# Optimization experiments

Hardware: AMD Instinct MI355X
Metric: run time of the kernel (lower is better)

Reference implementation:

```python
import jax, jax.numpy as jnp
import numpy as np

T, C, H, N = 1024, 2048, 32, 64
D_LORA, D_G = 64, 128

def _ln(x, w, b, eps=1e-5):
    m = x.mean(-1, keepdims=True)
    v = ((x - m) ** 2).mean(-1, keepdims=True)
    return (x - m) * jax.lax.rsqrt(v + eps) * w + b

def setup_inputs():
    key = jax.random.key(0)
    ks = iter(jax.random.split(key, 48))
    rn = lambda shape, s=1.0: jax.random.normal(next(ks), shape, dtype=jnp.float32) * s
    return {
        "x": rn((T, C)),
        "x_prev_att": rn((C,)),
        "vk_state": rn((H, N, N), 0.1),
        "x_prev_ffn": rn((C,)),
        "v_first": rn((T, C)),
        "ln1_w": jnp.ones((C,), jnp.float32), "ln1_b": jnp.zeros((C,), jnp.float32),
        "x_r": rn((C,), 0.1), "x_w": rn((C,), 0.1), "x_k": rn((C,), 0.1),
        "x_v": rn((C,), 0.1), "x_a": rn((C,), 0.1), "x_g": rn((C,), 0.1),
        "w0": rn((C,), 0.1), "w1": rn((C, D_LORA), 0.02), "w2": rn((D_LORA, C), 0.02),
        "a0": rn((C,), 0.1), "a1": rn((C, D_LORA), 0.02), "a2": rn((D_LORA, C), 0.02),
        "v0": rn((C,), 0.1), "v1": rn((C, D_LORA), 0.02), "v2": rn((D_LORA, C), 0.02),
        "g1": rn((C, D_G), 0.02), "g2": rn((D_G, C), 0.02),
        "k_k": rn((C,), 0.1), "k_a": rn((C,), 0.1), "r_k": rn((C,), 0.1),
        "R_": rn((C, C), 0.02), "K_": rn((C, C), 0.02),
        "V_": rn((C, C), 0.02), "O_": rn((C, C), 0.02),
        "lnx_w": jnp.ones((C,), jnp.float32), "lnx_b": jnp.zeros((C,), jnp.float32),
        "ln2_w": jnp.ones((C,), jnp.float32), "ln2_b": jnp.zeros((C,), jnp.float32),
        "ffn_x_k": rn((C,), 0.1),
        "ffn_K": rn((C, 4 * C), 0.02), "ffn_V": rn((4 * C, C), 0.02),
    }

def reference(x, x_prev_att, vk_state, x_prev_ffn, v_first, ln1_w, ln1_b,
              x_r, x_w, x_k, x_v, x_a, x_g, w0, w1, w2, a0, a1, a2,
              v0, v1, v2, g1, g2, k_k, k_a, r_k, R_, K_, V_, O_,
              lnx_w, lnx_b, ln2_w, ln2_b, ffn_x_k, ffn_K, ffn_V):
    # ---- TMix: RWKV-7 time mixing (layer_id = 1, so v_first blend is active) ----
    xln = _ln(x, ln1_w, ln1_b)                                  # [T, C]
    dx = jnp.concatenate([x_prev_att[None, :], xln[:-1]], axis=0) - xln  # token shift
    xr, xw, xk, xv, xa, xg = (xln + dx * m for m in (x_r, x_w, x_k, x_v, x_a, x_g))
    r = xr @ R_
    w = jnp.tanh(xw @ w1) @ w2
    k = xk @ K_
    v = xv @ V_
    a = jax.nn.sigmoid(a0 + (xa @ a1) @ a2)
    g = jax.nn.sigmoid(xg @ g1) @ g2
    kk = (k * k_k).reshape(T, H, N)
    kk = kk / jnp.maximum(jnp.linalg.norm(kk, axis=-1, keepdims=True), 1e-12)  # L2 normalize per head
    k = k * (1.0 + (a - 1.0) * k_a)
    v = v + (v_first - v) * jax.nn.sigmoid(v0 + (xv @ v1) @ v2)  # layer_id != 0 path
    w = jnp.exp(-0.606531 * jax.nn.sigmoid(w0 + w))               # per-channel decay in (0,1)
    rh, kh, vh = r.reshape(T, H, N), k.reshape(T, H, N), v.reshape(T, H, N)
    ah, wh = a.reshape(T, H, N), w.reshape(T, H, N)

    def step(state, inp):
        # state: [H, N, N]; generalized delta rule: state*w + state@(-kk)(kk*a)^T + v k^T
        w_t, kk_t, a_t, k_t, v_t, r_t = inp
        ab = jnp.einsum('hi,hj->hij', -kk_t, kk_t * a_t)
        vk = jnp.einsum('hi,hj->hij', v_t, k_t)
        state = state * w_t[:, None, :] + jnp.einsum('hij,hjk->hik', state, ab) + vk
        return state, jnp.einsum('hij,hj->hi', state, r_t)

    vk_state, outs = jax.lax.scan(step, vk_state, (wh, kk, ah, kh, vh, rh))  # outs: [T, H, N]
    # group norm over H groups, eps = 0.00064, affine per-channel
    m = outs.mean(-1, keepdims=True)
    var = ((outs - m) ** 2).mean(-1, keepdims=True)
    gn = ((outs - m) * jax.lax.rsqrt(var + 0.00064)).reshape(T, C) * lnx_w + lnx_b
    bonus = ((r * k * r_k).reshape(T, H, N).sum(-1, keepdims=True) * vh).reshape(T, C)
    x = x + ((gn + bonus) * g) @ O_
    # ---- CMix: gated squared-ReLU MLP ----
    xln2 = _ln(x, ln2_w, ln2_b)
    dx2 = jnp.concatenate([x_prev_ffn[None, :], xln2[:-1]], axis=0) - xln2
    kf = jax.nn.relu((xln2 + dx2 * ffn_x_k) @ ffn_K) ** 2
    x = x + kf @ ffn_V
    return x
```

## Files before the change

kernel.cpp:

```cpp
#include <hip/hip_runtime.h>
#include <hip/hip_bf16.h>


#define T_ 1024
#define C_ 2048
#define H_ 32
#define NH 64

typedef __attribute__((ext_vector_type(8))) short short8v;
typedef __attribute__((ext_vector_type(4))) float f32x4;

__device__ __forceinline__ float bf2f(unsigned short u) {
  union { float f; unsigned int i; } c; c.i = ((unsigned int)u) << 16; return c.f;
}
__device__ __forceinline__ unsigned short f2bf(float f) {
  union { float f; unsigned int i; } c; c.f = f;
  unsigned int x = c.i;
  return (unsigned short)((x + 0x7fffu + ((x >> 16) & 1u)) >> 16);
}
__device__ __forceinline__ float sigm(float x) { return 1.f / (1.f + __expf(-x)); }

__device__ __forceinline__ void load8bf(const unsigned short* p, float* o) {
  union { int4 v; unsigned short u[8]; } c;
  c.v = *(const int4*)p;
#pragma unroll
  for (int i = 0; i < 8; ++i) o[i] = bf2f(c.u[i]);
}
__device__ __forceinline__ void store8bf(unsigned short* p, const float* o) {
  union { int4 v; unsigned short u[8]; } c;
#pragma unroll
  for (int i = 0; i < 8; ++i) c.u[i] = f2bf(o[i]);
  *(int4*)p = c.v;
}
__device__ __forceinline__ void load8f(const float* p, float* o) {
  float4 a = ((const float4*)p)[0], b = ((const float4*)p)[1];
  o[0] = a.x; o[1] = a.y; o[2] = a.z; o[3] = a.w;
  o[4] = b.x; o[5] = b.y; o[6] = b.z; o[7] = b.w;
}
__device__ __forceinline__ void load4f(const float* p, float* o) {
  float4 a = *(const float4*)p;
  o[0] = a.x; o[1] = a.y; o[2] = a.z; o[3] = a.w;
}

#define GLD16(g, l)                                                        \
  __builtin_amdgcn_global_load_lds(                                        \
      (const __attribute__((address_space(1))) void*)(g),                  \
      (__attribute__((address_space(3))) void*)(l), 16, 0, 0)

__global__ __launch_bounds__(256) void lnmix6_kernel(
    const float* __restrict__ x, const float* __restrict__ xprev,
    const float* __restrict__ lw, const float* __restrict__ lb,
    const float* __restrict__ mr, const float* __restrict__ mw,
    const float* __restrict__ mk, const float* __restrict__ mv,
    const float* __restrict__ ma, const float* __restrict__ mg,
    unsigned short* xr, unsigned short* xw, unsigned short* xk,
    unsigned short* xv, unsigned short* xa, unsigned short* xg) {
  int t = blockIdx.x, tid = threadIdx.x, c = tid * 8;
  float cur[8], prv[8];
  load8f(x + (size_t)t * C_ + c, cur);
  if (t == 0) load8f(xprev + c, prv);
  else load8f(x + (size_t)(t - 1) * C_ + c, prv);
  float sc = 0.f, qc = 0.f, sp = 0.f, qp = 0.f;
#pragma unroll
  for (int i = 0; i < 8; ++i) {
    sc += cur[i]; qc += cur[i] * cur[i];
    sp += prv[i]; qp += prv[i] * prv[i];
  }
  for (int m = 1; m < 64; m <<= 1) {
    sc += __shfl_xor(sc, m); qc += __shfl_xor(qc, m);
    sp += __shfl_xor(sp, m); qp += __shfl_xor(qp, m);
  }
  __shared__ float r4[4][4];
  if ((tid & 63) == 0) {
    r4[tid >> 6][0] = sc; r4[tid >> 6][1] = qc;
    r4[tid >> 6][2] = sp; r4[tid >> 6][3] = qp;
  }
  __syncthreads();
  sc = r4[0][0] + r4[1][0] + r4[2][0] + r4[3][0];
  qc = r4[0][1] + r4[1][1] + r4[2][1] + r4[3][1];
  sp = r4[0][2] + r4[1][2] + r4[2][2] + r4[3][2];
  qp = r4[0][3] + r4[1][3] + r4[2][3] + r4[3][3];
  float mc = sc * (1.f / C_);
  float rc = rsqrtf(qc * (1.f / C_) - mc * mc + 1e-5f);
  float mp = sp * (1.f / C_);
  float rp = rsqrtf(qp * (1.f / C_) - mp * mp + 1e-5f);
  float cw[8], cb[8];
  load8f(lw + c, cw); load8f(lb + c, cb);
  float curn[8], prvn[8];
#pragma unroll
  for (int i = 0; i < 8; ++i) {
    curn[i] = (cur[i] - mc) * rc * cw[i] + cb[i];
    prvn[i] = (t == 0) ? prv[i] : (prv[i] - mp) * rp * cw[i] + cb[i];
  }
  float cf[8], o[8];
  const float* coefs[6] = {mr, mw, mk, mv, ma, mg};
  unsigned short* outs6[6] = {xr, xw, xk, xv, xa, xg};
#pragma unroll
  for (int a = 0; a < 6; ++a) {
    load8f(coefs[a] + c, cf);
#pragma unroll
    for (int i = 0; i < 8; ++i) o[i] = curn[i] + (prvn[i] - curn[i]) * cf[i];
    store8bf(outs6[a] + (size_t)t * C_ + c, o);
  }
}

__global__ __launch_bounds__(256) void lnmix1_kernel(
    const float* __restrict__ x, const float* __restrict__ xprev,
    const float* __restrict__ lw, const float* __restrict__ lb,
    const float* __restrict__ coef, unsigned short* __restrict__ out) {
  int t = blockIdx.x, tid = threadIdx.x, c = tid * 8;
  float cur[8], prv[8];
  load8f(x + (size_t)t * C_ + c, cur);
  if (t == 0) load8f(xprev + c, prv);
  else load8f(x + (size_t)(t - 1) * C_ + c, prv);
  float sc = 0.f, qc = 0.f, sp = 0.f, qp = 0.f;
#pragma unroll
  for (int i = 0; i < 8; ++i) {
    sc += cur[i]; qc += cur[i] * cur[i];
    sp += prv[i]; qp += prv[i] * prv[i];
  }
  for (int m = 1; m < 64; m <<= 1) {
    sc += __shfl_xor(sc, m); qc += __shfl_xor(qc, m);
    sp += __shfl_xor(sp, m); qp += __shfl_xor(qp, m);
  }
  __shared__ float r4[4][4];
  if ((tid & 63) == 0) {
    r4[tid >> 6][0] = sc; r4[tid >> 6][1] = qc;
    r4[tid >> 6][2] = sp; r4[tid >> 6][3] = qp;
  }
  __syncthreads();
  sc = r4[0][0] + r4[1][0] + r4[2][0] + r4[3][0];
  qc = r4[0][1] + r4[1][1] + r4[2][1] + r4[3][1];
  sp = r4[0][2] + r4[1][2] + r4[2][2] + r4[3][2];
  qp = r4[0][3] + r4[1][3] + r4[2][3] + r4[3][3];
  float mc = sc * (1.f / C_);
  float rc = rsqrtf(qc * (1.f / C_) - mc * mc + 1e-5f);
  float mp = sp * (1.f / C_);
  float rp = rsqrtf(qp * (1.f / C_) - mp * mp + 1e-5f);
  float cw[8], cb[8], cf[8], o[8];
  load8f(lw + c, cw); load8f(lb + c, cb); load8f(coef + c, cf);
#pragma unroll
  for (int i = 0; i < 8; ++i) {
    float cn = (cur[i] - mc) * rc * cw[i] + cb[i];
    float pn = (t == 0) ? prv[i] : (prv[i] - mp) * rp * cw[i] + cb[i];
    o[i] = cn + (pn - cn) * cf[i];
  }
  store8bf(out + (size_t)t * C_ + c, o);
}

__global__ __launch_bounds__(256) void transpose_kernel(
    const float* in0, const float* in1, const float* in2,
    unsigned short* o0, unsigned short* o1, unsigned short* o2,
    int R, int Cc) {
  const float* in = blockIdx.z == 0 ? in0 : (blockIdx.z == 1 ? in1 : in2);
  unsigned short* out = blockIdx.z == 0 ? o0 : (blockIdx.z == 1 ? o1 : o2);
  __shared__ __align__(16) unsigned short tile[64][80];
  int c0 = blockIdx.x * 64, r0 = blockIdx.y * 64;
  int rr = threadIdx.x >> 4, cq = threadIdx.x & 15;
#pragma unroll
  for (int i = 0; i < 4; ++i) {
    int r = rr + i * 16;
    float4 v = *(const float4*)(in + (size_t)(r0 + r) * Cc + c0 + cq * 4);
    tile[cq * 4 + 0][r] = f2bf(v.x);
    tile[cq * 4 + 1][r] = f2bf(v.y);
    tile[cq * 4 + 2][r] = f2bf(v.z);
    tile[cq * 4 + 3][r] = f2bf(v.w);
  }
  __syncthreads();
  int cr = threadIdx.x >> 2, rg = threadIdx.x & 3;
  int4 w0 = *(const int4*)&tile[cr][rg * 16];
  int4 w1 = *(const int4*)&tile[cr][rg * 16 + 8];
  unsigned short* op = out + (size_t)(c0 + cr) * R + r0 + rg * 16;
  *(int4*)op = w0;
  *(int4*)(op + 8) = w1;
}

template <int EPI>
__global__ __launch_bounds__(256) void gemm2_kernel(
    const unsigned short* A0, const unsigned short* A1, const unsigned short* A2,
    const unsigned short* B0, const unsigned short* B1, const unsigned short* B2,
    void* C0, void* C1, void* C2, const float* __restrict__ addsrc,
    int M, int K, int N) {
  int z = blockIdx.z;
  const unsigned short* A = z == 0 ? A0 : (z == 1 ? A1 : A2);
  const unsigned short* Bt = z == 0 ? B0 : (z == 1 ? B1 : B2);
  void* Cout = z == 0 ? C0 : (z == 1 ? C1 : C2);
  __shared__ __align__(16) unsigned short As[2][128 * 32];
  __shared__ __align__(16) unsigned short Bs[2][128 * 32];
  const int tid = threadIdx.x, lane = tid & 63, wid = tid >> 6;
  const int bm = blockIdx.y * 128, bn = blockIdx.x * 128;
  const int wr = wid >> 1, wc = wid & 1;
  const int mrow = lane & 15, krow = lane >> 4;
  auto stage = [&](int buf, int kt) {
#pragma unroll
    for (int q = 0; q < 2; ++q) {
      int s = q * 2048 + tid * 8;
      int m = s >> 5, k = s & 31;
      GLD16(A + (size_t)(bm + m) * K + kt + k, &As[buf][s]);
      GLD16(Bt + (size_t)(bn + m) * K + kt + k, &Bs[buf][s]);
    }
  };
  f32x4 acc[4][4] = {};
  stage(0, 0);
  __syncthreads();
  int buf = 0;
  for (int kt = 0; kt < K; kt += 32) {
    if (kt + 32 < K) stage(buf ^ 1, kt + 32);
    short8v af[4], bfrag[4];
#pragma unroll
    for (int i = 0; i < 4; ++i)
      af[i] = *(const short8v*)&As[buf][(wr * 64 + i * 16 + mrow) * 32 + krow * 8];
#pragma unroll
    for (int j = 0; j < 4; ++j)
      bfrag[j] = *(const short8v*)&Bs[buf][(wc * 64 + j * 16 + mrow) * 32 + krow * 8];
#pragma unroll
    for (int i = 0; i < 4; ++i)
#pragma unroll
      for (int j = 0; j < 4; ++j)
        acc[i][j] = __builtin_amdgcn_mfma_f32_16x16x32_bf16(af[i], bfrag[j], acc[i][j], 0, 0, 0);
    __syncthreads();
    buf ^= 1;
  }
#pragma unroll
  for (int i = 0; i < 4; ++i)
#pragma unroll
    for (int j = 0; j < 4; ++j)
#pragma unroll
      for (int e = 0; e < 4; ++e) {
        int grow = bm + wr * 64 + i * 16 + (lane >> 4) * 4 + e;
        int gcol = bn + wc * 64 + j * 16 + (lane & 15);
        size_t off = (size_t)grow * N + gcol;
        float v = acc[i][j][e];
        if constexpr (EPI == 0) ((float*)Cout)[off] = v;
        else if constexpr (EPI == 1) ((float*)Cout)[off] = addsrc[off] + v;
        else { float r = v > 0.f ? v : 0.f; ((unsigned short*)Cout)[off] = f2bf(r * r); }
      }
}

__global__ __launch_bounds__(256) void gemm2ks_kernel(
    const unsigned short* __restrict__ A, const unsigned short* __restrict__ Bt,
    unsigned short* __restrict__ P, int M, int KH, int Ktot, int N) {
  int kz = blockIdx.z;
  const size_t kbase = (size_t)kz * KH;
  __shared__ __align__(16) unsigned short As[2][128 * 32];
  __shared__ __align__(16) unsigned short Bs[2][128 * 32];
  const int tid = threadIdx.x, lane = tid & 63, wid = tid >> 6;
  const int bm = blockIdx.y * 128, bn = blockIdx.x * 128;
  const int wr = wid >> 1, wc = wid & 1;
  const int mrow = lane & 15, krow = lane >> 4;
  auto stage = [&](int buf, int kt) {
#pragma unroll
    for (int q = 0; q < 2; ++q) {
      int s = q * 2048 + tid * 8;
      int m = s >> 5, k = s & 31;
      GLD16(A + (size_t)(bm + m) * Ktot + kbase + kt + k, &As[buf][s]);
      GLD16(Bt + (size_t)(bn + m) * Ktot + kbase + kt + k, &Bs[buf][s]);
    }
  };
  f32x4 acc[4][4] = {};
  stage(0, 0);
  __syncthreads();
  int buf = 0;
  for (int kt = 0; kt < KH; kt += 32) {
    if (kt + 32 < KH) stage(buf ^ 1, kt + 32);
    short8v af[4], bfrag[4];
#pragma unroll
    for (int i = 0; i < 4; ++i)
      af[i] = *(const short8v*)&As[buf][(wr * 64 + i * 16 + mrow) * 32 + krow * 8];
#pragma unroll
    for (int j = 0; j < 4; ++j)
      bfrag[j] = *(const short8v*)&Bs[buf][(wc * 64 + j * 16 + mrow) * 32 + krow * 8];
#pragma unroll
    for (int i = 0; i < 4; ++i)
#pragma unroll
      for (int j = 0; j < 4; ++j)
        acc[i][j] = __builtin_amdgcn_mfma_f32_16x16x32_bf16(af[i], bfrag[j], acc[i][j], 0, 0, 0);
    __syncthreads();
    buf ^= 1;
  }
  unsigned short* Pz = P + (size_t)kz * M * N;
#pragma unroll
  for (int i = 0; i < 4; ++i)
#pragma unroll
    for (int j = 0; j < 4; ++j)
#pragma unroll
      for (int e = 0; e < 4; ++e) {
        int grow = bm + wr * 64 + i * 16 + (lane >> 4) * 4 + e;
        int gcol = bn + wc * 64 + j * 16 + (lane & 15);
        Pz[(size_t)grow * N + gcol] = f2bf(acc[i][j][e]);
      }
}

__global__ __launch_bounds__(256) void gemm2ks3_kernel(
    const unsigned short* A0, const unsigned short* A1, const unsigned short* A2,
    const unsigned short* B0, const unsigned short* B1, const unsigned short* B2,
    unsigned short* __restrict__ P, int M, int KH, int Ktot, int N) {
  int z = blockIdx.z;
  int batch = z % 3, kz = z / 3;
  const unsigned short* A = batch == 0 ? A0 : (batch == 1 ? A1 : A2);
  const unsigned short* Bt = batch == 0 ? B0 : (batch == 1 ? B1 : B2);
  const size_t kbase = (size_t)kz * KH;
  __shared__ __align__(16) unsigned short As[2][128 * 32];
  __shared__ __align__(16) unsigned short Bs[2][128 * 32];
  const int tid = threadIdx.x, lane = tid & 63, wid = tid >> 6;
  const int bm = blockIdx.y * 128, bn = blockIdx.x * 128;
  const int wr = wid >> 1, wc = wid & 1;
  const int mrow = lane & 15, krow = lane >> 4;
  auto stage = [&](int buf, int kt) {
#pragma unroll
    for (int q = 0; q < 2; ++q) {
      int s = q * 2048 + tid * 8;
      int m = s >> 5, k = s & 31;
      GLD16(A + (size_t)(bm + m) * Ktot + kbase + kt + k, &As[buf][s]);
      GLD16(Bt + (size_t)(bn + m) * Ktot + kbase + kt + k, &Bs[buf][s]);
    }
  };
  f32x4 acc[4][4] = {};
  stage(0, 0);
  __syncthreads();
  int buf = 0;
  for (int kt = 0; kt < KH; kt += 32) {
    if (kt + 32 < KH) stage(buf ^ 1, kt + 32);
    short8v af[4], bfrag[4];
#pragma unroll
    for (int i = 0; i < 4; ++i)
      af[i] = *(const short8v*)&As[buf][(wr * 64 + i * 16 + mrow) * 32 + krow * 8];
#pragma unroll
    for (int j = 0; j < 4; ++j)
      bfrag[j] = *(const short8v*)&Bs[buf][(wc * 64 + j * 16 + mrow) * 32 + krow * 8];
#pragma unroll
    for (int i = 0; i < 4; ++i)
#pragma unroll
      for (int j = 0; j < 4; ++j)
        acc[i][j] = __builtin_amdgcn_mfma_f32_16x16x32_bf16(af[i], bfrag[j], acc[i][j], 0, 0, 0);
    __syncthreads();
    buf ^= 1;
  }
  unsigned short* Pz = P + (size_t)z * M * N;
#pragma unroll
  for (int i = 0; i < 4; ++i)
#pragma unroll
    for (int j = 0; j < 4; ++j)
#pragma unroll
      for (int e = 0; e < 4; ++e) {
        int grow = bm + wr * 64 + i * 16 + (lane >> 4) * 4 + e;
        int gcol = bn + wc * 64 + j * 16 + (lane & 15);
        Pz[(size_t)grow * N + gcol] = f2bf(acc[i][j][e]);
      }
}

__global__ __launch_bounds__(256) void add5_kernel(
    const float* __restrict__ a, const unsigned short* __restrict__ p,
    float* __restrict__ o) {
  size_t i = ((size_t)blockIdx.x * 256 + threadIdx.x) * 8;
  const size_t TC = (size_t)T_ * C_;
  float va[8], v0[8], v1[8], v2[8], v3[8], r[8];
  load8f(a + i, va);
  load8bf(p + i, v0);
  load8bf(p + i + TC, v1);
  load8bf(p + i + 2 * TC, v2);
  load8bf(p + i + 3 * TC, v3);
#pragma unroll
  for (int k = 0; k < 8; ++k) r[k] = va[k] + v0[k] + v1[k] + v2[k] + v3[k];
  *(float4*)(o + i) = make_float4(r[0], r[1], r[2], r[3]);
  *(float4*)(o + i + 4) = make_float4(r[4], r[5], r[6], r[7]);
}

__global__ __launch_bounds__(256) void gemm_ks3_kernel(
    const unsigned short* A0, const unsigned short* A1, const unsigned short* A2,
    const unsigned short* B0, const unsigned short* B1, const unsigned short* B2,
    float* P0, float* P1, float* P2, int K, int N) {
  int mz = blockIdx.z >> 3, kz = blockIdx.z & 7;
  const unsigned short* A = mz == 0 ? A0 : (mz == 1 ? A1 : A2);
  const unsigned short* Bt = mz == 0 ? B0 : (mz == 1 ? B1 : B2);
  float* partial = mz == 0 ? P0 : (mz == 1 ? P1 : P2);
  __shared__ __align__(16) unsigned short As[2][128 * 32];
  __shared__ __align__(16) unsigned short Bs[2][64 * 32];
  const int tid = threadIdx.x, lane = tid & 63, wid = tid >> 6;
  const int bn = blockIdx.x * 64, bm = blockIdx.y * 128;
  const int wr = wid >> 1, wc = wid & 1;
  const int mrow = lane & 15, krow = lane >> 4;
  auto stage = [&](int buf, int kt) {
#pragma unroll
    for (int q = 0; q < 2; ++q) {
      int s = q * 2048 + tid * 8;
      int m = s >> 5, k = s & 31;
      GLD16(A + (size_t)(bm + m) * K + kt + k, &As[buf][s]);
    }
    {
      int s = tid * 8;
      int n = s >> 5, k = s & 31;
      GLD16(Bt + (size_t)(bn + n) * K + kt + k, &Bs[buf][s]);
    }
  };
  f32x4 acc[4][2] = {};
  int k0 = kz * 256;
  stage(0, k0);
  __syncthreads();
  int buf = 0;
  for (int kt = k0; kt < k0 + 256; kt += 32) {
    if (kt + 32 < k0 + 256) stage(buf ^ 1, kt + 32);
    short8v af[4], bfrag[2];
#pragma unroll
    for (int i = 0; i < 4; ++i)
      af[i] = *(const short8v*)&As[buf][(wr * 64 + i * 16 + mrow) * 32 + krow * 8];
#pragma unroll
    for (int j = 0; j < 2; ++j)
      bfrag[j] = *(const short8v*)&Bs[buf][(wc * 32 + j * 16 + mrow) * 32 + krow * 8];
#pragma unroll
    for (int i = 0; i < 4; ++i)
#pragma unroll
      for (int j = 0; j < 2; ++j)
        acc[i][j] = __builtin_amdgcn_mfma_f32_16x16x32_bf16(af[i], bfrag[j], acc[i][j], 0, 0, 0);
    __syncthreads();
    buf ^= 1;
  }
#pragma unroll
  for (int i = 0; i < 4; ++i)
#pragma unroll
    for (int j = 0; j < 2; ++j)
#pragma unroll
      for (int e = 0; e < 4; ++e) {
        int row = bm + wr * 64 + i * 16 + (lane >> 4) * 4 + e;
        int col = bn + wc * 32 + j * 16 + (lane & 15);
        partial[((size_t)kz * 1024 + row) * N + col] = acc[i][j][e];
      }
}

__global__ __launch_bounds__(256) void gemm_ks_kernel(
    const unsigned short* __restrict__ A, const unsigned short* __restrict__ Bt,
    float* __restrict__ partial, int K, int N) {
  __shared__ __align__(16) unsigned short As[2][128 * 32];
  __shared__ __align__(16) unsigned short Bs[2][64 * 32];
  const int tid = threadIdx.x, lane = tid & 63, wid = tid >> 6;
  const int bn = blockIdx.x * 64, bm = blockIdx.y * 128, kz = blockIdx.z;
  const int wr = wid >> 1, wc = wid & 1;
  const int mrow = lane & 15, krow = lane >> 4;
  auto stage = [&](int buf, int kt) {
#pragma unroll
    for (int q = 0; q < 2; ++q) {
      int s = q * 2048 + tid * 8;
      int m = s >> 5, k = s & 31;
      GLD16(A + (size_t)(bm + m) * K + kt + k, &As[buf][s]);
    }
    {
      int s = tid * 8;
      int n = s >> 5, k = s & 31;
      GLD16(Bt + (size_t)(bn + n) * K + kt + k, &Bs[buf][s]);
    }
  };
  f32x4 acc[4][2] = {};
  int k0 = kz * 256;
  stage(0, k0);
  __syncthreads();
  int buf = 0;
  for (int kt = k0; kt < k0 + 256; kt += 32) {
    if (kt + 32 < k0 + 256) stage(buf ^ 1, kt + 32);
    short8v af[4], bfrag[2];
#pragma unroll
    for (int i = 0; i < 4; ++i)
      af[i] = *(const short8v*)&As[buf][(wr * 64 + i * 16 + mrow) * 32 + krow * 8];
#pragma unroll
    for (int j = 0; j < 2; ++j)
      bfrag[j] = *(const short8v*)&Bs[buf][(wc * 32 + j * 16 + mrow) * 32 + krow * 8];
#pragma unroll
    for (int i = 0; i < 4; ++i)
#pragma unroll
      for (int j = 0; j < 2; ++j)
        acc[i][j] = __builtin_amdgcn_mfma_f32_16x16x32_bf16(af[i], bfrag[j], acc[i][j], 0, 0, 0);
    __syncthreads();
    buf ^= 1;
  }
#pragma unroll
  for (int i = 0; i < 4; ++i)
#pragma unroll
    for (int j = 0; j < 2; ++j)
#pragma unroll
      for (int e = 0; e < 4; ++e) {
        int row = bm + wr * 64 + i * 16 + (lane >> 4) * 4 + e;
        int col = bn + wc * 32 + j * 16 + (lane & 15);
        partial[((size_t)kz * 1024 + row) * N + col] = acc[i][j][e];
      }
}

__global__ __launch_bounds__(128) void lora_combine_kernel(
    const float* __restrict__ pw, const float* __restrict__ pa,
    const float* __restrict__ pv, const float* __restrict__ pg,
    unsigned short* __restrict__ hw, unsigned short* __restrict__ ha,
    unsigned short* __restrict__ hv, unsigned short* __restrict__ hg) {
  int t = blockIdx.x, which = blockIdx.y, tid = threadIdx.x;
  int Nl = (which == 3) ? 128 : 64;
  if (tid >= Nl) return;
  const float* p = which == 0 ? pw : which == 1 ? pa : which == 2 ? pv : pg;
  float s = 0.f;
#pragma unroll
  for (int kz = 0; kz < 8; ++kz) s += p[((size_t)kz * 1024 + t) * Nl + tid];
  float r = which == 0 ? tanhf(s) : (which == 3 ? sigm(s) : s);
  unsigned short* o = which == 0 ? hw : which == 1 ? ha : which == 2 ? hv : hg;
  o[t * Nl + tid] = f2bf(r);
}

__global__ __launch_bounds__(256) void post_kernel(
    const unsigned short* __restrict__ qRKV, const float* __restrict__ wpre,
    const float* __restrict__ apre, const float* __restrict__ vpre,
    const float* __restrict__ vfirst, const float* __restrict__ w0,
    const float* __restrict__ a0, const float* __restrict__ v0_,
    const float* __restrict__ k_k, const float* __restrict__ k_a,
    float* __restrict__ scanin) {
  int t = blockIdx.x, tid = threadIdx.x;
  int c = tid * 8, h = tid >> 3, j = c & 63;
  size_t o = (size_t)t * C_ + c;
  const size_t TC = (size_t)T_ * C_;
  float rv[8], kv[8], vv[8], t0[8], wv[8], av[8], vp[8], vf[8];
  load8bf(qRKV + o, rv);          load8bf(qRKV + 3 * TC + o, t0);
#pragma unroll
  for (int i = 0; i < 8; ++i) rv[i] += t0[i];
  load8bf(qRKV + TC + o, kv);     load8bf(qRKV + 4 * TC + o, t0);
#pragma unroll
  for (int i = 0; i < 8; ++i) kv[i] += t0[i];
  load8bf(qRKV + 2 * TC + o, vv); load8bf(qRKV + 5 * TC + o, t0);
#pragma unroll
  for (int i = 0; i < 8; ++i) vv[i] += t0[i];
  load8f(wpre + o, wv); load8f(apre + o, av); load8f(vpre + o, vp);
  load8f(vfirst + o, vf);
  float ckk[8], cka[8], cw0[8], ca0[8], cv0[8];
  load8f(k_k + c, ckk); load8f(k_a + c, cka); load8f(w0 + c, cw0);
  load8f(a0 + c, ca0); load8f(v0_ + c, cv0);
  float kk[8]; float ss = 0.f;
#pragma unroll
  for (int i = 0; i < 8; ++i) { kk[i] = kv[i] * ckk[i]; ss += kk[i] * kk[i]; }
  ss += __shfl_xor(ss, 1); ss += __shfl_xor(ss, 2); ss += __shfl_xor(ss, 4);
  float rdn = 1.f / fmaxf(sqrtf(ss), 1e-12f);
  float sw[8], skn[8], scc[8], sk2[8], sv[8];
#pragma unroll
  for (int i = 0; i < 8; ++i) {
    float kkn = kk[i] * rdn;
    float a = sigm(ca0[i] + av[i]);
    skn[i] = kkn;
    scc[i] = -kkn * a;
    sk2[i] = kv[i] * (1.f + (a - 1.f) * cka[i]);
    float sg = sigm(cv0[i] + vp[i]);
    sv[i] = vv[i] + (vf[i] - vv[i]) * sg;
    sw[i] = __expf(-0.606531f * sigm(cw0[i] + wv[i]));
  }
  float* bp = scanin + ((size_t)h * T_ + t) * 384 + j;
  ((float4*)(bp + 0))[0]   = make_float4(sw[0], sw[1], sw[2], sw[3]);
  ((float4*)(bp + 4))[0]   = make_float4(sw[4], sw[5], sw[6], sw[7]);
  ((float4*)(bp + 64))[0]  = make_float4(skn[0], skn[1], skn[2], skn[3]);
  ((float4*)(bp + 68))[0]  = make_float4(skn[4], skn[5], skn[6], skn[7]);
  ((float4*)(bp + 128))[0] = make_float4(scc[0], scc[1], scc[2], scc[3]);
  ((float4*)(bp + 132))[0] = make_float4(scc[4], scc[5], scc[6], scc[7]);
  ((float4*)(bp + 192))[0] = make_float4(sk2[0], sk2[1], sk2[2], sk2[3]);
  ((float4*)(bp + 196))[0] = make_float4(sk2[4], sk2[5], sk2[6], sk2[7]);
  ((float4*)(bp + 256))[0] = make_float4(sv[0], sv[1], sv[2], sv[3]);
  ((float4*)(bp + 260))[0] = make_float4(sv[4], sv[5], sv[6], sv[7]);
  ((float4*)(bp + 320))[0] = make_float4(rv[0], rv[1], rv[2], rv[3]);
  ((float4*)(bp + 324))[0] = make_float4(rv[4], rv[5], rv[6], rv[7]);
}

struct SR { float wv[4], nv[4], cv[4], kv[4], rv[4], vvv; };

template <int CTRL>
__device__ __forceinline__ float dppadd(float x) {
  int y = __builtin_amdgcn_update_dpp(0, __float_as_int(x), CTRL, 0xF, 0xF, true);
  return x + __int_as_float(y);
}
__device__ __forceinline__ float red16(float x) {
  x = dppadd<0xB1>(x);
  x = dppadd<0x4E>(x);
  x = dppadd<0x140>(x);
  x = dppadd<0x141>(x);
  return x;
}

__device__ __forceinline__ void loadstep(const float* S, SR& R, int p4, int row) {
  load4f(S + p4, R.wv);
  load4f(S + 64 + p4, R.nv);
  load4f(S + 128 + p4, R.cv);
  load4f(S + 192 + p4, R.kv);
  load4f(S + 320 + p4, R.rv);
  R.vvv = S[256 + row];
}

__device__ __forceinline__ void stepcomp(const SR& R, float* st, int part,
                                         float* __restrict__ ob, size_t oidx) {
  float p0 = fmaf(st[0], R.nv[0], 0.f);
  float p1 = fmaf(st[1], R.nv[1], 0.f);
  p0 = fmaf(st[2], R.nv[2], p0);
  p1 = fmaf(st[3], R.nv[3], p1);
  float sa = red16(p0 + p1);
  float s0 = 0.f, s1 = 0.f;
#pragma unroll
  for (int i = 0; i < 4; ++i) {
    float t = fmaf(st[i], R.wv[i], fmaf(sa, R.cv[i], R.vvv * R.kv[i]));
    st[i] = t;
    if (i & 1) s1 = fmaf(t, R.rv[i], s1);
    else s0 = fmaf(t, R.rv[i], s0);
  }
  float so = red16(s0 + s1);
  if (part == 0) ob[oidx] = so;
}

__global__ __launch_bounds__(64) void scan5_kernel(
    const float* __restrict__ scanin, const float* __restrict__ vk0,
    float* __restrict__ outs) {
  int bid = blockIdx.x;
  int h = (bid & 7) + 8 * ((bid >> 3) & 3);
  int rg = bid >> 5;
  int tid = threadIdx.x;
  int part = tid & 15, row = rg * 4 + (tid >> 4);
  int p4 = part * 4;
  float st[4];
  load4f(vk0 + ((size_t)h * NH + row) * NH + p4, st);
  const float* src = scanin + (size_t)h * T_ * 384;
  float* ob = outs + h * NH + row;
  SR A, B, C, D;
  loadstep(src + 0 * 384, A, p4, row);
  loadstep(src + 1 * 384, B, p4, row);
  loadstep(src + 2 * 384, C, p4, row);
  int s = 0;
  for (; s < T_ - 4; s += 4) {
    const float* sp = src + (size_t)s * 384;
    loadstep(sp + 3 * 384, D, p4, row);
    stepcomp(A, st, part, ob, (size_t)(s + 0) * C_);
    loadstep(sp + 4 * 384, A, p4, row);
    stepcomp(B, st, part, ob, (size_t)(s + 1) * C_);
    loadstep(sp + 5 * 384, B, p4, row);
    stepcomp(C, st, part, ob, (size_t)(s + 2) * C_);
    loadstep(sp + 6 * 384, C, p4, row);
    stepcomp(D, st, part, ob, (size_t)(s + 3) * C_);
  }
  loadstep(src + (size_t)(T_ - 1) * 384, D, p4, row);
  stepcomp(A, st, part, ob, (size_t)(s + 0) * C_);
  stepcomp(B, st, part, ob, (size_t)(s + 1) * C_);
  stepcomp(C, st, part, ob, (size_t)(s + 2) * C_);
  stepcomp(D, st, part, ob, (size_t)(s + 3) * C_);
}

__global__ __launch_bounds__(256) void gnb_kernel(
    const float* __restrict__ outs, const float* __restrict__ scanin,
    const float* __restrict__ g, const float* __restrict__ rk,
    const float* __restrict__ gw, const float* __restrict__ gb,
    unsigned short* __restrict__ attin) {
  int t = blockIdx.x, tid = threadIdx.x;
  int c = tid * 8, h = tid >> 3, j = c & 63;
  float o[8], gv[8], rkv[8];
  load8f(outs + (size_t)t * C_ + c, o);
  load8f(g + (size_t)t * C_ + c, gv);
  load8f(rk + c, rkv);
  size_t sbase = ((size_t)h * T_ + t) * 384 + j;
  float rv[8], k2[8], vv[8];
  load8f(scanin + sbase + 320, rv);
  load8f(scanin + sbase + 192, k2);
  load8f(scanin + sbase + 256, vv);
  float s = 0.f, q = 0.f, bs = 0.f;
#pragma unroll
  for (int i = 0; i < 8; ++i) {
    s += o[i]; q += o[i] * o[i];
    bs += rv[i] * k2[i] * rkv[i];
  }
  s += __shfl_xor(s, 1); s += __shfl_xor(s, 2); s += __shfl_xor(s, 4);
  q += __shfl_xor(q, 1); q += __shfl_xor(q, 2); q += __shfl_xor(q, 4);
  bs += __shfl_xor(bs, 1); bs += __shfl_xor(bs, 2); bs += __shfl_xor(bs, 4);
  float mean = s * (1.f / NH);
  float var = q * (1.f / NH) - mean * mean;
  float rstd = rsqrtf(var + 0.00064f);
  float res[8];
#pragma unroll
  for (int i = 0; i < 8; ++i) {
    float gn = (o[i] - mean) * rstd * gw[c + i] + gb[c + i];
    res[i] = (gn + bs * vv[i]) * gv[i];
  }
  store8bf(attin + (size_t)t * C_ + c, res);
}

extern "C" void kernel_launch(void* const* d_in, const int* in_sizes, int n_in,
                              void* d_out, int out_size, void* d_ws, size_t ws_size,
                              hipStream_t stream) {
  const float* x       = (const float*)d_in[0];
  const float* xprev_a = (const float*)d_in[1];
  const float* vk0     = (const float*)d_in[2];
  const float* xprev_f = (const float*)d_in[3];
  const float* vfirst  = (const float*)d_in[4];
  const float* ln1w = (const float*)d_in[5];
  const float* ln1b = (const float*)d_in[6];
  const float* m_r = (const float*)d_in[7];
  const float* m_w = (const float*)d_in[8];
  const float* m_k = (const float*)d_in[9];
  const float* m_v = (const float*)d_in[10];
  const float* m_a = (const float*)d_in[11];
  const float* m_g = (const float*)d_in[12];
  const float* w0 = (const float*)d_in[13];
  const float* w1 = (const float*)d_in[14];
  const float* w2 = (const float*)d_in[15];
  const float* a0 = (const float*)d_in[16];
  const float* a1 = (const float*)d_in[17];
  const float* a2 = (const float*)d_in[18];
  const float* v0 = (const float*)d_in[19];
  const float* v1 = (const float*)d_in[20];
  const float* v2 = (const float*)d_in[21];
  const float* g1 = (const float*)d_in[22];
  const float* g2 = (const float*)d_in[23];
  const float* k_k = (const float*)d_in[24];
  const float* k_a = (const float*)d_in[25];
  const float* r_k = (const float*)d_in[26];
  const float* R_ = (const float*)d_in[27];
  const float* K_ = (const float*)d_in[28];
  const float* V_ = (const float*)d_in[29];
  const float* O_ = (const float*)d_in[30];
  const float* lnxw = (const float*)d_in[31];
  const float* lnxb = (const float*)d_in[32];
  const float* ln2w = (const float*)d_in[33];
  const float* ln2b = (const float*)d_in[34];
  const float* fxk = (const float*)d_in[35];
  const float* fK = (const float*)d_in[36];
  const float* fV = (const float*)d_in[37];
  float* out = (float*)d_out;

  char* ws = (char*)d_ws;
  const size_t MB = 1ull << 20;
  unsigned short* attin = (unsigned short*)(ws + 0 * MB);
  unsigned short* xr    = (unsigned short*)(ws + 4 * MB);
  unsigned short* xw    = (unsigned short*)(ws + 8 * MB);
  unsigned short* xkf   = (unsigned short*)(ws + 8 * MB);
  unsigned short* xk    = (unsigned short*)(ws + 12 * MB);
  unsigned short* xv    = (unsigned short*)(ws + 16 * MB);
  unsigned short* xa    = (unsigned short*)(ws + 20 * MB);
  unsigned short* xg    = (unsigned short*)(ws + 24 * MB);
  float* wpre  = (float*)(ws + 4 * MB);
  float* apre  = (float*)(ws + 12 * MB);
  float* vpre  = (float*)(ws + 20 * MB);
  unsigned short* qRKV = (unsigned short*)(ws + 28 * MB);
  unsigned short* fVt = (unsigned short*)(ws + 28 * MB);
  float* outsb = (float*)(ws + 52 * MB);
  float* x_att = (float*)(ws + 60 * MB);
  float* g_buf = (float*)(ws + 76 * MB);
  float* scanin = (float*)(ws + 84 * MB);
  unsigned short* Rt  = (unsigned short*)(ws + 84 * MB);
  unsigned short* Kt  = (unsigned short*)(ws + 92 * MB);
  unsigned short* Vt  = (unsigned short*)(ws + 100 * MB);
  unsigned short* Ot  = (unsigned short*)(ws + 84 * MB);
  unsigned short* qO  = (unsigned short*)(ws + 92 * MB);
  unsigned short* hffn = (unsigned short*)(ws + 84 * MB);
  unsigned short* fKt  = (unsigned short*)(ws + 100 * MB);
  unsigned short* pF   = (unsigned short*)(ws + 4 * MB);
  unsigned short* w1t = (unsigned short*)(ws + 0);
  unsigned short* a1t = (unsigned short*)(ws + 262144);
  unsigned short* v1t = (unsigned short*)(ws + 524288);
  unsigned short* g1t = (unsigned short*)(ws + 786432);
  unsigned short* w2t = (unsigned short*)(ws + 0);
  unsigned short* a2t = (unsigned short*)(ws + 262144);
  unsigned short* v2t = (unsigned short*)(ws + 524288);
  unsigned short* g2t = (unsigned short*)(ws + 786432);
  unsigned short* hwb = (unsigned short*)(ws + 1376256);
  unsigned short* hab = (unsigned short*)(ws + 1507328);
  unsigned short* hvb = (unsigned short*)(ws + 1638400);
  unsigned short* hgb = (unsigned short*)(ws + 1769472);
  float* pw = (float*)(ws + 2 * MB);
  float* pa = (float*)(ws + 4 * MB);
  float* pv = (float*)(ws + 6 * MB);
  float* pg = (float*)(ws + 8 * MB);

  lnmix6_kernel<<<T_, 256, 0, stream>>>(x, xprev_a, ln1w, ln1b,
                                        m_r, m_w, m_k, m_v, m_a, m_g,
                                        xr, xw, xk, xv, xa, xg);
  transpose_kernel<<<dim3(32, 32, 3), 256, 0, stream>>>(R_, K_, V_, Rt, Kt, Vt, C_, C_);
  gemm2ks3_kernel<<<dim3(16, 8, 6), 256, 0, stream>>>(xr, xk, xv, Rt, Kt, Vt,
                                                      qRKV, T_, 1024, C_, C_);
  transpose_kernel<<<dim3(1, 32, 3), 256, 0, stream>>>(w1, a1, v1, w1t, a1t, v1t, C_, 64);
  transpose_kernel<<<dim3(2, 32, 1), 256, 0, stream>>>(g1, g1, g1, g1t, g1t, g1t, C_, 128);
  gemm_ks3_kernel<<<dim3(1, 8, 24), 256, 0, stream>>>(xw, xa, xv, w1t, a1t, v1t,
                                                      pw, pa, pv, C_, 64);
  gemm_ks_kernel<<<dim3(2, 8, 8), 256, 0, stream>>>(xg, g1t, pg, C_, 128);
  lora_combine_kernel<<<dim3(T_, 4), 128, 0, stream>>>(pw, pa, pv, pg, hwb, hab, hvb, hgb);
  transpose_kernel<<<dim3(32, 1, 3), 256, 0, stream>>>(w2, a2, v2, w2t, a2t, v2t, 64, C_);
  transpose_kernel<<<dim3(32, 2, 1), 256, 0, stream>>>(g2, g2, g2, g2t, g2t, g2t, 128, C_);
  gemm2_kernel<0><<<dim3(16, 8, 3), 256, 0, stream>>>(hwb, hab, hvb, w2t, a2t, v2t,
                                                      wpre, apre, vpre, nullptr, T_, 64, C_);
  gemm2_kernel<0><<<dim3(16, 8, 1), 256, 0, stream>>>(hgb, hgb, hgb, g2t, g2t, g2t,
                                                      g_buf, g_buf, g_buf, nullptr, T_, 128, C_);
  post_kernel<<<T_, 256, 0, stream>>>(qRKV, wpre, apre, vpre, vfirst,
                                      w0, a0, v0, k_k, k_a, scanin);
  scan5_kernel<<<512, 64, 0, stream>>>(scanin, vk0, outsb);
  gnb_kernel<<<T_, 256, 0, stream>>>(outsb, scanin, g_buf, r_k, lnxw, lnxb, attin);
  transpose_kernel<<<dim3(32, 32, 1), 256, 0, stream>>>(O_, O_, O_, Ot, Ot, Ot, C_, C_);
  transpose_kernel<<<dim3(32, 128, 1), 256, 0, stream>>>(fV, fV, fV, fVt, fVt, fVt, 4 * C_, C_);
  gemm2ks_kernel<<<dim3(16, 8, 4), 256, 0, stream>>>(attin, Ot, qO, T_, 512, C_, C_);
  add5_kernel<<<1024, 256, 0, stream>>>(x, qO, x_att);
  lnmix1_kernel<<<T_, 256, 0, stream>>>(x_att, xprev_f, ln2w, ln2b, fxk, xkf);
  transpose_kernel<<<dim3(128, 32, 1), 256, 0, stream>>>(fK, fK, fK, fKt, fKt, fKt, C_, 4 * C_);
  gemm2_kernel<2><<<dim3(64, 8, 1), 256, 0, stream>>>(xkf, xkf, xkf, fKt, fKt, fKt,
                                                      hffn, hffn, hffn, nullptr, T_, C_, 4 * C_);
  gemm2ks_kernel<<<dim3(16, 8, 4), 256, 0, stream>>>(hffn, fVt, pF, T_, 2048, 4 * C_, C_);
  add5_kernel<<<1024, 256, 0, stream>>>(x_att, pF, out);
}
```

Measured before the change: 470.8 us.

## Overlap weight transposes with the scan and residual-add kernels

The O and FFN-V weight transposes move into the scan launch as extra blocks, and the FFN-K transpose moves into the residual-add launch as extra blocks. The aim is to use idle compute units during the serial scan and to hide the bandwidth-heavy transposes, while also removing three kernel launches. Workspace buffers are reassigned to avoid aliasing between the concurrent work. The risk is that scan blocks now launch with 256 threads, 192 of them idle, under a changed launch bound, and share memory bandwidth with the transposes. Either could slow the latency-critical scan.

```diff
diff --git a/kernel.cpp b/kernel.cpp
--- a/kernel.cpp
+++ b/kernel.cpp
@@ -148,6 +148,29 @@
   store8bf(out + (size_t)t * C_ + c, o);
 }
 
+__device__ __forceinline__ void transpose_tile(
+    const float* __restrict__ in, unsigned short* __restrict__ out,
+    int R, int Cc, int bx, int by, unsigned short (*tile)[80]) {
+  int c0 = bx * 64, r0 = by * 64;
+  int rr = threadIdx.x >> 4, cq = threadIdx.x & 15;
+#pragma unroll
+  for (int i = 0; i < 4; ++i) {
+    int r = rr + i * 16;
+    float4 v = *(const float4*)(in + (size_t)(r0 + r) * Cc + c0 + cq * 4);
+    tile[cq * 4 + 0][r] = f2bf(v.x);
+    tile[cq * 4 + 1][r] = f2bf(v.y);
+    tile[cq * 4 + 2][r] = f2bf(v.z);
+    tile[cq * 4 + 3][r] = f2bf(v.w);
+  }
+  __syncthreads();
+  int cr = threadIdx.x >> 2, rg = threadIdx.x & 3;
+  int4 w0 = *(const int4*)&tile[cr][rg * 16];
+  int4 w1 = *(const int4*)&tile[cr][rg * 16 + 8];
+  unsigned short* op = out + (size_t)(c0 + cr) * R + r0 + rg * 16;
+  *(int4*)op = w0;
+  *(int4*)(op + 8) = w1;
+}
+
 __global__ __launch_bounds__(256) void transpose_kernel(
     const float* in0, const float* in1, const float* in2,
     unsigned short* o0, unsigned short* o1, unsigned short* o2,
@@ -155,24 +178,7 @@
   const float* in = blockIdx.z == 0 ? in0 : (blockIdx.z == 1 ? in1 : in2);
   unsigned short* out = blockIdx.z == 0 ? o0 : (blockIdx.z == 1 ? o1 : o2);
   __shared__ __align__(16) unsigned short tile[64][80];
-  int c0 = blockIdx.x * 64, r0 = blockIdx.y * 64;
-  int rr = threadIdx.x >> 4, cq = threadIdx.x & 15;
-#pragma unroll
-  for (int i = 0; i < 4; ++i) {
-    int r = rr + i * 16;
-    float4 v = *(const float4*)(in + (size_t)(r0 + r) * Cc + c0 + cq * 4);
-    tile[cq * 4 + 0][r] = f2bf(v.x);
-    tile[cq * 4 + 1][r] = f2bf(v.y);
-    tile[cq * 4 + 2][r] = f2bf(v.z);
-    tile[cq * 4 + 3][r] = f2bf(v.w);
-  }
-  __syncthreads();
-  int cr = threadIdx.x >> 2, rg = threadIdx.x & 3;
-  int4 w0 = *(const int4*)&tile[cr][rg * 16];
-  int4 w1 = *(const int4*)&tile[cr][rg * 16 + 8];
-  unsigned short* op = out + (size_t)(c0 + cr) * R + r0 + rg * 16;
-  *(int4*)op = w0;
-  *(int4*)(op + 8) = w1;
+  transpose_tile(in, out, R, Cc, blockIdx.x, blockIdx.y, tile);
 }
 
 template <int EPI>
@@ -364,6 +370,31 @@
   for (int k = 0; k < 8; ++k) r[k] = va[k] + v0[k] + v1[k] + v2[k] + v3[k];
   *(float4*)(o + i) = make_float4(r[0], r[1], r[2], r[3]);
   *(float4*)(o + i + 4) = make_float4(r[4], r[5], r[6], r[7]);
+}
+
+__global__ __launch_bounds__(256) void add5tr_kernel(
+    const float* __restrict__ a, const unsigned short* __restrict__ p,
+    float* __restrict__ o, const float* __restrict__ fK,
+    unsigned short* __restrict__ fKt) {
+  int bid = blockIdx.x;
+  if (bid < 1024) {
+    size_t i = ((size_t)bid * 256 + threadIdx.x) * 8;
+    const size_t TC = (size_t)T_ * C_;
+    float va[8], v0[8], v1[8], v2[8], v3[8], r[8];
+    load8f(a + i, va);
+    load8bf(p + i, v0);
+    load8bf(p + i + TC, v1);
+    load8bf(p + i + 2 * TC, v2);
+    load8bf(p + i + 3 * TC, v3);
+#pragma unroll
+    for (int k = 0; k < 8; ++k) r[k] = va[k] + v0[k] + v1[k] + v2[k] + v3[k];
+    *(float4*)(o + i) = make_float4(r[0], r[1], r[2], r[3]);
+    *(float4*)(o + i + 4) = make_float4(r[4], r[5], r[6], r[7]);
+    return;
+  }
+  __shared__ __align__(16) unsigned short tile[64][80];
+  int idx = bid - 1024;
+  transpose_tile(fK, fKt, C_, 4 * C_, idx & 127, idx >> 7, tile);
 }
 
 __global__ __launch_bounds__(256) void gemm_ks3_kernel(
@@ -601,10 +632,20 @@
   if (part == 0) ob[oidx] = so;
 }
 
-__global__ __launch_bounds__(64) void scan5_kernel(
+__global__ __launch_bounds__(256) void scanfuse_kernel(
     const float* __restrict__ scanin, const float* __restrict__ vk0,
-    float* __restrict__ outs) {
+    float* __restrict__ outs,
+    const float* __restrict__ Osrc, unsigned short* __restrict__ Ot,
+    const float* __restrict__ fVsrc, unsigned short* __restrict__ fVt) {
   int bid = blockIdx.x;
+  if (bid >= 512) {
+    __shared__ __align__(16) unsigned short tile[64][80];
+    int idx = bid - 512;
+    if (idx < 1024) transpose_tile(Osrc, Ot, C_, C_, idx & 31, idx >> 5, tile);
+    else { idx -= 1024; transpose_tile(fVsrc, fVt, 4 * C_, C_, idx & 31, idx >> 5, tile); }
+    return;
+  }
+  if (threadIdx.x >= 64) return;
   int h = (bid & 7) + 8 * ((bid >> 3) & 3);
   int rg = bid >> 5;
   int tid = threadIdx.x;
@@ -722,7 +763,6 @@
   unsigned short* attin = (unsigned short*)(ws + 0 * MB);
   unsigned short* xr    = (unsigned short*)(ws + 4 * MB);
   unsigned short* xw    = (unsigned short*)(ws + 8 * MB);
-  unsigned short* xkf   = (unsigned short*)(ws + 8 * MB);
   unsigned short* xk    = (unsigned short*)(ws + 12 * MB);
   unsigned short* xv    = (unsigned short*)(ws + 16 * MB);
   unsigned short* xa    = (unsigned short*)(ws + 20 * MB);
@@ -730,20 +770,21 @@
   float* wpre  = (float*)(ws + 4 * MB);
   float* apre  = (float*)(ws + 12 * MB);
   float* vpre  = (float*)(ws + 20 * MB);
+  unsigned short* fVt = (unsigned short*)(ws + 4 * MB);
+  unsigned short* xkf = (unsigned short*)(ws + 36 * MB);
   unsigned short* qRKV = (unsigned short*)(ws + 28 * MB);
-  unsigned short* fVt = (unsigned short*)(ws + 28 * MB);
   float* outsb = (float*)(ws + 52 * MB);
+  unsigned short* Ot = (unsigned short*)(ws + 60 * MB);
   float* x_att = (float*)(ws + 60 * MB);
   float* g_buf = (float*)(ws + 76 * MB);
   float* scanin = (float*)(ws + 84 * MB);
   unsigned short* Rt  = (unsigned short*)(ws + 84 * MB);
   unsigned short* Kt  = (unsigned short*)(ws + 92 * MB);
   unsigned short* Vt  = (unsigned short*)(ws + 100 * MB);
-  unsigned short* Ot  = (unsigned short*)(ws + 84 * MB);
-  unsigned short* qO  = (unsigned short*)(ws + 92 * MB);
+  unsigned short* qO  = (unsigned short*)(ws + 84 * MB);
   unsigned short* hffn = (unsigned short*)(ws + 84 * MB);
   unsigned short* fKt  = (unsigned short*)(ws + 100 * MB);
-  unsigned short* pF   = (unsigned short*)(ws + 4 * MB);
+  unsigned short* pF   = (unsigned short*)(ws + 100 * MB);
   unsigned short* w1t = (unsigned short*)(ws + 0);
   unsigned short* a1t = (unsigned short*)(ws + 262144);
   unsigned short* v1t = (unsigned short*)(ws + 524288);
@@ -781,14 +822,11 @@
                                                       g_buf, g_buf, g_buf, nullptr, T_, 128, C_);
   post_kernel<<<T_, 256, 0, stream>>>(qRKV, wpre, apre, vpre, vfirst,
                                       w0, a0, v0, k_k, k_a, scanin);
-  scan5_kernel<<<512, 64, 0, stream>>>(scanin, vk0, outsb);
+  scanfuse_kernel<<<5632, 256, 0, stream>>>(scanin, vk0, outsb, O_, Ot, fV, fVt);
   gnb_kernel<<<T_, 256, 0, stream>>>(outsb, scanin, g_buf, r_k, lnxw, lnxb, attin);
-  transpose_kernel<<<dim3(32, 32, 1), 256, 0, stream>>>(O_, O_, O_, Ot, Ot, Ot, C_, C_);
-  transpose_kernel<<<dim3(32, 128, 1), 256, 0, stream>>>(fV, fV, fV, fVt, fVt, fVt, 4 * C_, C_);
   gemm2ks_kernel<<<dim3(16, 8, 4), 256, 0, stream>>>(attin, Ot, qO, T_, 512, C_, C_);
-  add5_kernel<<<1024, 256, 0, stream>>>(x, qO, x_att);
+  add5tr_kernel<<<5120, 256, 0, stream>>>(x, qO, x_att, fK, fKt);
   lnmix1_kernel<<<T_, 256, 0, stream>>>(x_att, xprev_f, ln2w, ln2b, fxk, xkf);
-  transpose_kernel<<<dim3(128, 32, 1), 256, 0, stream>>>(fK, fK, fK, fKt, fKt, fKt, C_, 4 * C_);
   gemm2_kernel<2><<<dim3(64, 8, 1), 256, 0, stream>>>(xkf, xkf, xkf, fKt, fKt, fKt,
                                                       hffn, hffn, hffn, nullptr, T_, C_, 4 * C_);
   gemm2ks_kernel<<<dim3(16, 8, 4), 256, 0, stream>>>(hffn, fVt, pF, T_, 2048, 4 * C_, C_);
```

Measured after the change: 451.2 us. -4.2%, faster.
